# Kernel optimization log

Measured on AMD Instinct MI355X. Metric: run time of the kernel, lower is better.

The kernel has to match this reference:

```python
import jax, jax.numpy as jnp
import numpy as np

H = 12  # num_heads (init kwarg)


def setup_inputs() -> dict:
    key = jax.random.key(0)
    ks = jax.random.split(key, 9)
    B, S, D, M = 2, 1025, 768, 4
    hw = S - 1
    x = jax.random.normal(ks[0], (B, S, D), dtype=jnp.float32)
    masks = jax.random.randint(ks[1], (B, M, hw), 0, 2, dtype=jnp.int32)
    init = lambda k: jax.random.normal(k, (D, D), dtype=jnp.float32) * 0.02
    return {
        'x': x, 'masks': masks,
        'Wq': init(ks[2]), 'bq': jnp.zeros((D,), jnp.float32),
        'Wk': init(ks[3]), 'bk': jnp.zeros((D,), jnp.float32),
        'Wv': init(ks[4]), 'bv': jnp.zeros((D,), jnp.float32),
    }


def reference(x, masks, Wq, bq, Wk, bk, Wv, bv):
    B, S, D = x.shape
    hd = D // H
    scale = 1.0 / jnp.sqrt(jnp.asarray(hd, x.dtype))

    def heads(t):  # (B,S,D) -> (B,H,S,hd)
        return t.reshape(B, S, H, hd).transpose(0, 2, 1, 3)

    q = heads(x @ Wq.T + bq)
    k = heads(x @ Wk.T + bk)
    v = heads(x @ Wv.T + bv)

    scores_ori = jnp.einsum('bhqd,bhkd->bhqk', q, k) * scale  # (B,H,S,S)
    attn = jax.nn.softmax(scores_ori, axis=-1)  # dropout is identity at eval
    h = jnp.einsum('bhqk,bhkd->bhqd', attn, v)
    h = h.transpose(0, 2, 1, 3).reshape(B, S, D)

    # ---- mask-expanded attention (torch.no_grad branch) ----
    Mk, hw = masks.shape[1], masks.shape[2]
    m = masks.astype(x.dtype)  # (B,M,hw)
    # pad: position 0 (CLS) gets 0, positions 1..hw get the mask
    new_masks = jnp.pad(m, ((0, 0), (0, 0), (1, S - 1 - hw)))  # (B,M,S)
    bias = -10000.0 * (1.0 - new_masks)  # additive mask bias
    new_scores = scores_ori[:, None] + bias[:, :, None, None, :]  # (B,M,H,S,S)
    new_attn = jax.nn.softmax(new_scores, axis=-1)
    new_h = jnp.einsum('bmhqk,bhkd->bmhqd', new_attn, v)  # v repeated per mask
    new_h = new_h.transpose(0, 1, 3, 2, 4).reshape(B * Mk, S, D)

    img_idx = jnp.repeat(jnp.arange(B), Mk)  # [0]*M + [1]*M + ...
    new_x = jnp.broadcast_to(x[:, None], (B, Mk, S, D)).reshape(B * Mk, S, D)
    return (h, new_h, img_idx, new_x)
```

## Files before the change

kernel.cpp:

```cpp
#include <hip/hip_runtime.h>

typedef float f32x4 __attribute__((ext_vector_type(4)));
typedef short s16x8 __attribute__((ext_vector_type(8)));

constexpr int B  = 2;
constexpr int S  = 1025;
constexpr int D  = 768;
constexpr int DD = D * D;
constexpr int H  = 12;
constexpr int NM = 4;
constexpr int ROWS = B * S;
constexpr int BSD  = B * S * D;
constexpr int KPAD = 1088;
constexpr int NHB  = B * H;
constexpr int NQT  = 65;
constexpr int NKT  = 17;
constexpr int NV5  = 5;
constexpr int NATT = NHB * NQT;
constexpr int NCPY = 512;
constexpr int OUT_NEWH_OFF = BSD;
constexpr int OUT_IDX_OFF  = BSD + NM * BSD;
constexpr int OUT_NEWX_OFF = OUT_IDX_OFF + B * NM;

#define QSCALE 0.18033688011112042f

constexpr size_t QF_SZ = (size_t)NHB * NQT * 2 * 512;
constexpr size_t KF_SZ = (size_t)NHB * NKT * 4 * 2 * 512;
constexpr size_t VF_SZ = KF_SZ;

__device__ __forceinline__ unsigned short f2bf(float f) {
    unsigned u = __builtin_bit_cast(unsigned, f);
    u += 0x7FFF + ((u >> 16) & 1);
    return (unsigned short)(u >> 16);
}

__device__ __forceinline__ void gll16(const void* g, void* l) {
    __builtin_amdgcn_global_load_lds(
        (const __attribute__((address_space(1))) void*)g,
        (__attribute__((address_space(3))) void*)l, 16, 0, 0);
}

__global__ __launch_bounds__(256) void conv_kernel(
    const float* __restrict__ x, const float* __restrict__ Wq,
    const float* __restrict__ Wk, const float* __restrict__ Wv,
    const int* __restrict__ masks,
    unsigned short* __restrict__ xb, unsigned short* __restrict__ Wb,
    unsigned short* __restrict__ Mmb,
    unsigned short* __restrict__ Qf, unsigned short* __restrict__ Kf,
    unsigned short* __restrict__ Vf)
{
    constexpr int NX8 = BSD / 8;
    constexpr int NW8 = DD / 8;
    constexpr int TOT = NX8 + 3 * NW8;
    const int stride = gridDim.x * 256;
    const int tid = blockIdx.x * 256 + threadIdx.x;
    for (int c = tid; c < TOT; c += stride) {
        const float* src;
        unsigned short* dst;
        if (c < NX8) { src = x + (size_t)c * 8; dst = xb + (size_t)c * 8; }
        else {
            const int cc = c - NX8;
            const int mt = cc / NW8;
            const int rr = cc - mt * NW8;
            src = ((mt == 0) ? Wq : (mt == 1) ? Wk : Wv) + (size_t)rr * 8;
            dst = Wb + (size_t)mt * DD + (size_t)rr * 8;
        }
        const float4 a = *(const float4*)src;
        const float4 b2 = *(const float4*)(src + 4);
        s16x8 v;
        v[0] = (short)f2bf(a.x);  v[1] = (short)f2bf(a.y);
        v[2] = (short)f2bf(a.z);  v[3] = (short)f2bf(a.w);
        v[4] = (short)f2bf(b2.x); v[5] = (short)f2bf(b2.y);
        v[6] = (short)f2bf(b2.z); v[7] = (short)f2bf(b2.w);
        *(s16x8*)dst = v;
    }
    if (tid < B * NV5 * KPAD) {
        const int k    = tid % KPAD;
        const int rest = tid / KPAD;
        const int vv   = rest % NV5;
        const int bb   = rest / NV5;
        unsigned short m;
        if (vv == 0) m = (k < S) ? 0xFFFFu : 0u;
        else m = (k >= 1 && k < S &&
                  masks[(size_t)(bb * NM + vv - 1) * (S - 1) + k - 1]) ? 0xFFFFu : 0u;
        Mmb[tid] = m;
    }
    constexpr int KZ = NHB * 8 * 512;
    for (int i = tid; i < KZ; i += stride) {
        const int hb = i >> 12, off = i & 4095;
        Kf[(((size_t)(hb * NKT + NKT - 1)) << 12) + off] = 0;
        Vf[(((size_t)(hb * NKT + NKT - 1)) << 12) + off] = 0;
    }
    constexpr int QZ = NHB * 2 * 512;
    for (int i = tid; i < QZ; i += stride) {
        const int hb = i >> 10, off = i & 1023;
        Qf[(((size_t)(hb * NQT + NQT - 1) * 2) << 9) + off] = 0;
    }
}

__global__ __launch_bounds__(256, 2) void qkv_mfma_kernel(
    const unsigned short* __restrict__ xb, const unsigned short* __restrict__ Wb,
    const float* __restrict__ bq, const float* __restrict__ bk,
    const float* __restrict__ bv,
    unsigned short* __restrict__ Qf, unsigned short* __restrict__ Kf,
    unsigned short* __restrict__ Vf)
{
    __shared__ __align__(16) unsigned short Xs[2][128 * 64];
    __shared__ __align__(16) unsigned short Wl[2][128 * 64];

    const int t = threadIdx.x;
    const int row0 = blockIdx.x * 128;
    const int cy = blockIdx.y;
    const int mt = cy / 6;
    const int col0 = (cy % 6) * 128;
    const float* bias = (mt == 0) ? bq : (mt == 1) ? bk : bv;
    const unsigned short* Wsrc = Wb + (size_t)mt * DD;

    const int w = t >> 6, l = t & 63, lq = l & 15, grp = l >> 4;
    const int wr = w >> 1, wc = w & 1;

    auto stage = [&](int buf, int k0) {
        #pragma unroll
        for (int i = 0; i < 4; ++i) {
            const int slot = i * 256 + t;
            const int r = slot >> 3, cl = slot & 7;
            const int cg = cl ^ (r & 7);
            int row = row0 + r; if (row > ROWS - 1) row = ROWS - 1;
            gll16(xb + (size_t)row * D + k0 + cg * 8, &Xs[buf][slot * 8]);
            gll16(Wsrc + (size_t)(col0 + r) * D + k0 + cg * 8, &Wl[buf][slot * 8]);
        }
    };

    f32x4 acc[4][4] = {};
    stage(0, 0);

    for (int ks = 0; ks < 12; ++ks) {
        const int cur = ks & 1;
        __syncthreads();
        if (ks + 1 < 12) stage(cur ^ 1, (ks + 1) * 64);

        s16x8 a[4][2], bf[4][2];
        #pragma unroll
        for (int i = 0; i < 4; ++i) {
            const int xr = wr * 64 + i * 16 + lq;
            #pragma unroll
            for (int kh = 0; kh < 2; ++kh)
                a[i][kh] = *(const s16x8*)&Xs[cur][xr * 64 + (((kh * 4 + grp) ^ (xr & 7)) * 8)];
        }
        #pragma unroll
        for (int j = 0; j < 4; ++j) {
            const int wrow = wc * 64 + j * 16 + lq;
            #pragma unroll
            for (int kh = 0; kh < 2; ++kh)
                bf[j][kh] = *(const s16x8*)&Wl[cur][wrow * 64 + (((kh * 4 + grp) ^ (wrow & 7)) * 8)];
        }
        #pragma unroll
        for (int i = 0; i < 4; ++i)
            #pragma unroll
            for (int j = 0; j < 4; ++j) {
                acc[i][j] = __builtin_amdgcn_mfma_f32_16x16x32_bf16(a[i][0], bf[j][0], acc[i][j], 0, 0, 0);
                acc[i][j] = __builtin_amdgcn_mfma_f32_16x16x32_bf16(a[i][1], bf[j][1], acc[i][j], 0, 0, 0);
            }
    }

    #pragma unroll
    for (int j = 0; j < 4; ++j) {
        const int col = col0 + wc * 64 + j * 16 + lq;
        const float bv_ = bias[col];
        #pragma unroll
        for (int i = 0; i < 4; ++i) {
            #pragma unroll
            for (int r = 0; r < 4; ++r) {
                const int row = row0 + wr * 64 + i * 16 + grp * 4 + r;
                if (row >= ROWS) continue;
                const float raw = acc[i][j][r] + bv_;
                const int bb = (row >= S) ? 1 : 0;
                const int s  = row - bb * S;
                const int hb2 = bb * H + (col >> 6);
                const int d   = col & 63;
                if (mt == 0) {
                    const size_t idx = (((size_t)(hb2 * NQT + (s >> 4)) * 2 + (d >> 5)) << 9)
                                     + (((((d >> 3) & 3) << 4) + (s & 15)) << 3) + (d & 7);
                    Qf[idx] = f2bf(raw * QSCALE);
                } else if (mt == 1) {
                    const size_t idx = ((((size_t)(hb2 * NKT + (s >> 6)) * 4 + ((s >> 4) & 3)) * 2 + (d >> 5)) << 9)
                                     + (((((d >> 3) & 3) << 4) + (s & 15)) << 3) + (d & 7);
                    Kf[idx] = f2bf(raw);
                } else {
                    const int kk = s & 63;
                    const size_t idx = ((((size_t)(hb2 * NKT + (s >> 6)) * 4 + (d >> 4)) * 2 + (kk >> 5)) << 9)
                                     + (((((kk >> 3) & 3) << 4) + (d & 15)) << 3) + (kk & 7);
                    Vf[idx] = f2bf(raw);
                }
            }
        }
    }
}

__global__ __launch_bounds__(384) void attn_mfma_kernel(
    const unsigned short* __restrict__ Qf, const unsigned short* __restrict__ Kf,
    const unsigned short* __restrict__ Vf, const unsigned short* __restrict__ Mmb,
    const float* __restrict__ x,
    float* __restrict__ out_h, float* __restrict__ out_newh,
    float* __restrict__ out_newx, float* __restrict__ out_idx)
{
    if (blockIdx.x >= NATT) {
        const int cb = blockIdx.x - NATT;
        const int SLAB4  = S * D / 4;
        const int TOTAL4 = B * NM * SLAB4;
        const float4* x4 = (const float4*)x;
        float4* o4 = (float4*)out_newx;
        for (int f = cb * 384 + threadIdx.x; f < TOTAL4; f += NCPY * 384) {
            const int bm  = f / SLAB4;
            const int rem = f - bm * SLAB4;
            o4[f] = x4[(bm >> 2) * SLAB4 + rem];
        }
        if (cb == 0 && threadIdx.x < B * NM)
            out_idx[threadIdx.x] = (float)(threadIdx.x >> 2);
        return;
    }

    __shared__ __align__(16) unsigned short KVl[2][2][4096];
    __shared__ __align__(16) unsigned short Pb2[2][1024];

    const int orig = blockIdx.x;
    const int wgid = (orig & 7) * 195 + (orig >> 3);
    const int hb = wgid / NQT;
    const int qt = wgid - hb * NQT;
    const int b  = hb / H, hh = hb - b * H;
    const int q0 = qt * 16;

    const int t = threadIdx.x;
    const int w = t >> 6, l = t & 63;
    const int lq = l & 15, grp = l >> 4;

    const unsigned short* kfT = Kf + (((size_t)(hb * NKT)) << 12);
    const unsigned short* vfT = Vf + (((size_t)(hb * NKT)) << 12);

    auto stage = [&](int buf, int tile) {
        const unsigned short* ks = kfT + ((size_t)tile << 12);
        const unsigned short* vs = vfT + ((size_t)tile << 12);
        #pragma unroll
        for (int i = 0; i < 3; ++i) {
            const int s = t + i * 384;
            if (s < 512)       gll16(ks + s * 8, &KVl[buf][0][s * 8]);
            else if (s < 1024) gll16(vs + (s - 512) * 8, &KVl[buf][1][(s - 512) * 8]);
        }
    };

    stage(0, 0);

    if (w == 0) {
        s16x8 qf0, qf1;
        {
            const unsigned short* p = Qf + (((size_t)(hb * NQT + qt) * 2) << 9) + (l << 3);
            qf0 = *(const s16x8*)p;
            qf1 = *(const s16x8*)(p + 512);
        }
        #pragma unroll
        for (int it = 0; it < NKT; ++it) {
            const int cur = it & 1;
            __syncthreads();
            if (it + 1 < NKT) stage(cur ^ 1, it + 1);

            s16x8 kf[4][2];
            #pragma unroll
            for (int kt = 0; kt < 4; ++kt)
                #pragma unroll
                for (int kh = 0; kh < 2; ++kh)
                    kf[kt][kh] = *(const s16x8*)&KVl[cur][0][((kt * 2 + kh) << 9) + l * 8];

            f32x4 qk[4] = {};
            __builtin_amdgcn_s_setprio(1);
            #pragma unroll
            for (int kt = 0; kt < 4; ++kt) {
                qk[kt] = __builtin_amdgcn_mfma_f32_16x16x32_bf16(kf[kt][0], qf0, qk[kt], 0, 0, 0);
                qk[kt] = __builtin_amdgcn_mfma_f32_16x16x32_bf16(kf[kt][1], qf1, qk[kt], 0, 0, 0);
            }
            __builtin_amdgcn_s_setprio(0);

            unsigned short* P = &Pb2[cur][0];
            #pragma unroll
            for (int kt = 0; kt < 4; ++kt) {
                float e0, e1, e2, e3;
                asm("v_exp_f32 %0, %1" : "=v"(e0) : "v"(qk[kt][0]));
                asm("v_exp_f32 %0, %1" : "=v"(e1) : "v"(qk[kt][1]));
                asm("v_exp_f32 %0, %1" : "=v"(e2) : "v"(qk[kt][2]));
                asm("v_exp_f32 %0, %1" : "=v"(e3) : "v"(qk[kt][3]));
                unsigned d0, d1;
                asm("v_cvt_pk_bf16_f32 %0, %1, %2" : "=v"(d0) : "v"(e0), "v"(e1));
                asm("v_cvt_pk_bf16_f32 %0, %1, %2" : "=v"(d1) : "v"(e2), "v"(e3));
                const int chunk = kt * 2 + (grp >> 1);
                *(uint2*)&P[lq * 64 + ((chunk ^ (lq & 7)) * 8) + (grp & 1) * 4] =
                    make_uint2(d0, d1);
            }
        }
        __syncthreads();
    } else {
        const int vv = w - 1;
        const unsigned short* mbase = Mmb + (size_t)(b * NV5 + vv) * KPAD + grp * 8;

        s16x8 onesf;
        #pragma unroll
        for (int i = 0; i < 8; ++i) onesf[i] = (short)0x3F80;

        f32x4 acc[5] = {};
        s16x8 vfp[4][2];

        auto pv = [&](s16x8 ea0, s16x8 ea1, int mi) {
            s16x8 mm0 = *(const s16x8*)(mbase + mi * 64);
            s16x8 mm1 = *(const s16x8*)(mbase + mi * 64 + 32);
            s16x8 pa0 = ea0 & mm0;
            s16x8 pa1 = ea1 & mm1;
            __builtin_amdgcn_s_setprio(1);
            #pragma unroll
            for (int dt = 0; dt < 4; ++dt)
                acc[dt] = __builtin_amdgcn_mfma_f32_16x16x32_bf16(vfp[dt][0], pa0, acc[dt], 0, 0, 0);
            acc[4] = __builtin_amdgcn_mfma_f32_16x16x32_bf16(onesf, pa0, acc[4], 0, 0, 0);
            #pragma unroll
            for (int dt = 0; dt < 4; ++dt)
                acc[dt] = __builtin_amdgcn_mfma_f32_16x16x32_bf16(vfp[dt][1], pa1, acc[dt], 0, 0, 0);
            acc[4] = __builtin_amdgcn_mfma_f32_16x16x32_bf16(onesf, pa1, acc[4], 0, 0, 0);
            __builtin_amdgcn_s_setprio(0);
        };

        #pragma unroll
        for (int it = 0; it < NKT; ++it) {
            const int cur = it & 1;
            __syncthreads();
            if (it + 1 < NKT) stage(cur ^ 1, it + 1);

            s16x8 pr0, pr1;
            if (it > 0) {
                const unsigned short* Pr = &Pb2[cur ^ 1][0];
                pr0 = *(const s16x8*)&Pr[lq * 64 + ((grp ^ (lq & 7)) * 8)];
                pr1 = *(const s16x8*)&Pr[lq * 64 + (((4 + grp) ^ (lq & 7)) * 8)];
            }
            s16x8 vfc[4][2];
            #pragma unroll
            for (int dt = 0; dt < 4; ++dt)
                #pragma unroll
                for (int kh = 0; kh < 2; ++kh)
                    vfc[dt][kh] = *(const s16x8*)&KVl[cur][1][((dt * 2 + kh) << 9) + l * 8];

            if (it > 0) pv(pr0, pr1, it - 1);

            #pragma unroll
            for (int dt = 0; dt < 4; ++dt) {
                vfp[dt][0] = vfc[dt][0];
                vfp[dt][1] = vfc[dt][1];
            }
        }
        __syncthreads();
        {
            const unsigned short* Pr = &Pb2[(NKT - 1) & 1][0];
            s16x8 pr0 = *(const s16x8*)&Pr[lq * 64 + ((grp ^ (lq & 7)) * 8)];
            s16x8 pr1 = *(const s16x8*)&Pr[lq * 64 + (((4 + grp) ^ (lq & 7)) * 8)];
            pv(pr0, pr1, NKT - 1);
        }

        const int q = q0 + lq;
        if (q < S) {
            const float inv = 1.0f / acc[4][0];
            float* bp = ((vv == 0)
                ? out_h    + (size_t)(b * S + q) * D
                : out_newh + (size_t)((b * NM + vv - 1) * S + q) * D) + hh * 64 + grp * 4;
            #pragma unroll
            for (int dt = 0; dt < 4; ++dt) {
                float4 s4;
                s4.x = acc[dt][0] * inv; s4.y = acc[dt][1] * inv;
                s4.z = acc[dt][2] * inv; s4.w = acc[dt][3] * inv;
                *(float4*)(bp + dt * 16) = s4;
            }
        }
    }
}

extern "C" void kernel_launch(void* const* d_in, const int* in_sizes, int n_in,
                              void* d_out, int out_size, void* d_ws, size_t ws_size,
                              hipStream_t stream)
{
    const float* x     = (const float*)d_in[0];
    const int*   masks = (const int*)  d_in[1];
    const float* Wq    = (const float*)d_in[2];
    const float* bq    = (const float*)d_in[3];
    const float* Wk    = (const float*)d_in[4];
    const float* bk    = (const float*)d_in[5];
    const float* Wv    = (const float*)d_in[6];
    const float* bv    = (const float*)d_in[7];

    float* out = (float*)d_out;
    float* out_h    = out;
    float* out_newh = out + OUT_NEWH_OFF;
    float* out_idx  = out + OUT_IDX_OFF;
    float* out_newx = out + OUT_NEWX_OFF;

    unsigned short* Qf  = (unsigned short*)d_ws;
    unsigned short* Kf  = Qf + QF_SZ;
    unsigned short* Vf  = Kf + KF_SZ;
    unsigned short* Mmb = Vf + VF_SZ;

    unsigned short* xb = (unsigned short*)out_newx;
    unsigned short* Wb = xb + BSD;

    conv_kernel<<<1634, 256, 0, stream>>>(x, Wq, Wk, Wv, masks, xb, Wb, Mmb,
                                          Qf, Kf, Vf);
    {
        dim3 grid(17, 18);
        qkv_mfma_kernel<<<grid, 256, 0, stream>>>(xb, Wb, bq, bk, bv, Qf, Kf, Vf);
    }
    attn_mfma_kernel<<<NATT + NCPY, 384, 0, stream>>>(Qf, Kf, Vf, Mmb, x,
                                                      out_h, out_newh,
                                                      out_newx, out_idx);
}
```

Before: 96.71 us.

## Split PV work by head-dim slice per wave, loading V fragments directly from global

Waves 1-4 each compute one 16-wide slice of the head dimension for all five mask variants, instead of each wave computing the full head dimension for one variant. A dedicated wave 5 computes the row sums for all variants and publishes them through shared memory. V is no longer staged in LDS; each wave reads its own V fragments straight from global memory, which halves the staged LDS traffic. The row sums now need an extra barrier, and the V loads become uncached global reads on the critical path.

```diff
diff --git a/kernel.cpp b/kernel.cpp
--- a/kernel.cpp
+++ b/kernel.cpp
@@ -220,8 +220,9 @@
         return;
     }
 
-    __shared__ __align__(16) unsigned short KVl[2][2][4096];
+    __shared__ __align__(16) unsigned short Kl[2][4096];
     __shared__ __align__(16) unsigned short Pb2[2][1024];
+    __shared__ float Ssum[NV5][16];
 
     const int orig = blockIdx.x;
     const int wgid = (orig & 7) * 195 + (orig >> 3);
@@ -235,16 +236,13 @@
     const int lq = l & 15, grp = l >> 4;
 
     const unsigned short* kfT = Kf + (((size_t)(hb * NKT)) << 12);
-    const unsigned short* vfT = Vf + (((size_t)(hb * NKT)) << 12);
 
     auto stage = [&](int buf, int tile) {
         const unsigned short* ks = kfT + ((size_t)tile << 12);
-        const unsigned short* vs = vfT + ((size_t)tile << 12);
-        #pragma unroll
-        for (int i = 0; i < 3; ++i) {
+        #pragma unroll
+        for (int i = 0; i < 2; ++i) {
             const int s = t + i * 384;
-            if (s < 512)       gll16(ks + s * 8, &KVl[buf][0][s * 8]);
-            else if (s < 1024) gll16(vs + (s - 512) * 8, &KVl[buf][1][(s - 512) * 8]);
+            if (s < 512) gll16(ks + s * 8, &Kl[buf][s * 8]);
         }
     };
 
@@ -257,25 +255,20 @@
             qf0 = *(const s16x8*)p;
             qf1 = *(const s16x8*)(p + 512);
         }
-        #pragma unroll
+        #pragma unroll 1
         for (int it = 0; it < NKT; ++it) {
             const int cur = it & 1;
             __syncthreads();
             if (it + 1 < NKT) stage(cur ^ 1, it + 1);
 
-            s16x8 kf[4][2];
-            #pragma unroll
-            for (int kt = 0; kt < 4; ++kt)
-                #pragma unroll
-                for (int kh = 0; kh < 2; ++kh)
-                    kf[kt][kh] = *(const s16x8*)&KVl[cur][0][((kt * 2 + kh) << 9) + l * 8];
-
             f32x4 qk[4] = {};
             __builtin_amdgcn_s_setprio(1);
             #pragma unroll
             for (int kt = 0; kt < 4; ++kt) {
-                qk[kt] = __builtin_amdgcn_mfma_f32_16x16x32_bf16(kf[kt][0], qf0, qk[kt], 0, 0, 0);
-                qk[kt] = __builtin_amdgcn_mfma_f32_16x16x32_bf16(kf[kt][1], qf1, qk[kt], 0, 0, 0);
+                s16x8 k0v = *(const s16x8*)&Kl[cur][((kt * 2 + 0) << 9) + l * 8];
+                s16x8 k1v = *(const s16x8*)&Kl[cur][((kt * 2 + 1) << 9) + l * 8];
+                qk[kt] = __builtin_amdgcn_mfma_f32_16x16x32_bf16(k0v, qf0, qk[kt], 0, 0, 0);
+                qk[kt] = __builtin_amdgcn_mfma_f32_16x16x32_bf16(k1v, qf1, qk[kt], 0, 0, 0);
             }
             __builtin_amdgcn_s_setprio(0);
 
@@ -296,35 +289,16 @@
             }
         }
         __syncthreads();
-    } else {
-        const int vv = w - 1;
-        const unsigned short* mbase = Mmb + (size_t)(b * NV5 + vv) * KPAD + grp * 8;
-
-        s16x8 onesf;
-        #pragma unroll
-        for (int i = 0; i < 8; ++i) onesf[i] = (short)0x3F80;
-
-        f32x4 acc[5] = {};
-        s16x8 vfp[4][2];
-
-        auto pv = [&](s16x8 ea0, s16x8 ea1, int mi) {
-            s16x8 mm0 = *(const s16x8*)(mbase + mi * 64);
-            s16x8 mm1 = *(const s16x8*)(mbase + mi * 64 + 32);
-            s16x8 pa0 = ea0 & mm0;
-            s16x8 pa1 = ea1 & mm1;
-            __builtin_amdgcn_s_setprio(1);
-            #pragma unroll
-            for (int dt = 0; dt < 4; ++dt)
-                acc[dt] = __builtin_amdgcn_mfma_f32_16x16x32_bf16(vfp[dt][0], pa0, acc[dt], 0, 0, 0);
-            acc[4] = __builtin_amdgcn_mfma_f32_16x16x32_bf16(onesf, pa0, acc[4], 0, 0, 0);
-            #pragma unroll
-            for (int dt = 0; dt < 4; ++dt)
-                acc[dt] = __builtin_amdgcn_mfma_f32_16x16x32_bf16(vfp[dt][1], pa1, acc[dt], 0, 0, 0);
-            acc[4] = __builtin_amdgcn_mfma_f32_16x16x32_bf16(onesf, pa1, acc[4], 0, 0, 0);
-            __builtin_amdgcn_s_setprio(0);
-        };
-
-        #pragma unroll
+        __syncthreads();
+    } else if (w <= 4) {
+        const int dt = w - 1;
+        const unsigned short* mball = Mmb + (size_t)(b * NV5) * KPAD + grp * 8;
+        const unsigned short* vfb = Vf + (((size_t)(hb * NKT)) << 12) + (l << 3);
+
+        f32x4 acc[NV5] = {};
+        s16x8 vfp0, vfp1;
+
+        #pragma unroll 1
         for (int it = 0; it < NKT; ++it) {
             const int cur = it & 1;
             __syncthreads();
@@ -336,43 +310,101 @@
                 pr0 = *(const s16x8*)&Pr[lq * 64 + ((grp ^ (lq & 7)) * 8)];
                 pr1 = *(const s16x8*)&Pr[lq * 64 + (((4 + grp) ^ (lq & 7)) * 8)];
             }
-            s16x8 vfc[4][2];
-            #pragma unroll
-            for (int dt = 0; dt < 4; ++dt)
+            s16x8 nv0 = *(const s16x8*)&vfb[((size_t)(it * 8 + dt * 2 + 0)) << 9];
+            s16x8 nv1 = *(const s16x8*)&vfb[((size_t)(it * 8 + dt * 2 + 1)) << 9];
+
+            if (it > 0) {
+                const int mi = it - 1;
+                __builtin_amdgcn_s_setprio(1);
                 #pragma unroll
-                for (int kh = 0; kh < 2; ++kh)
-                    vfc[dt][kh] = *(const s16x8*)&KVl[cur][1][((dt * 2 + kh) << 9) + l * 8];
-
-            if (it > 0) pv(pr0, pr1, it - 1);
-
-            #pragma unroll
-            for (int dt = 0; dt < 4; ++dt) {
-                vfp[dt][0] = vfc[dt][0];
-                vfp[dt][1] = vfc[dt][1];
-            }
+                for (int v = 0; v < NV5; ++v) {
+                    s16x8 mm0 = *(const s16x8*)(mball + (size_t)v * KPAD + mi * 64);
+                    s16x8 mm1 = *(const s16x8*)(mball + (size_t)v * KPAD + mi * 64 + 32);
+                    acc[v] = __builtin_amdgcn_mfma_f32_16x16x32_bf16(vfp0, pr0 & mm0, acc[v], 0, 0, 0);
+                    acc[v] = __builtin_amdgcn_mfma_f32_16x16x32_bf16(vfp1, pr1 & mm1, acc[v], 0, 0, 0);
+                }
+                __builtin_amdgcn_s_setprio(0);
+            }
+            vfp0 = nv0; vfp1 = nv1;
         }
         __syncthreads();
         {
-            const unsigned short* Pr = &Pb2[(NKT - 1) & 1][0];
+            const int mi = NKT - 1;
+            const unsigned short* Pr = &Pb2[mi & 1][0];
             s16x8 pr0 = *(const s16x8*)&Pr[lq * 64 + ((grp ^ (lq & 7)) * 8)];
             s16x8 pr1 = *(const s16x8*)&Pr[lq * 64 + (((4 + grp) ^ (lq & 7)) * 8)];
-            pv(pr0, pr1, NKT - 1);
-        }
+            #pragma unroll
+            for (int v = 0; v < NV5; ++v) {
+                s16x8 mm0 = *(const s16x8*)(mball + (size_t)v * KPAD + mi * 64);
+                s16x8 mm1 = *(const s16x8*)(mball + (size_t)v * KPAD + mi * 64 + 32);
+                acc[v] = __builtin_amdgcn_mfma_f32_16x16x32_bf16(vfp0, pr0 & mm0, acc[v], 0, 0, 0);
+                acc[v] = __builtin_amdgcn_mfma_f32_16x16x32_bf16(vfp1, pr1 & mm1, acc[v], 0, 0, 0);
+            }
+        }
+        __syncthreads();
 
         const int q = q0 + lq;
         if (q < S) {
-            const float inv = 1.0f / acc[4][0];
-            float* bp = ((vv == 0)
-                ? out_h    + (size_t)(b * S + q) * D
-                : out_newh + (size_t)((b * NM + vv - 1) * S + q) * D) + hh * 64 + grp * 4;
-            #pragma unroll
-            for (int dt = 0; dt < 4; ++dt) {
+            #pragma unroll
+            for (int v = 0; v < NV5; ++v) {
+                const float inv = 1.0f / Ssum[v][lq];
+                float* bp = ((v == 0)
+                    ? out_h    + (size_t)(b * S + q) * D
+                    : out_newh + (size_t)((b * NM + v - 1) * S + q) * D)
+                    + hh * 64 + dt * 16 + grp * 4;
                 float4 s4;
-                s4.x = acc[dt][0] * inv; s4.y = acc[dt][1] * inv;
-                s4.z = acc[dt][2] * inv; s4.w = acc[dt][3] * inv;
-                *(float4*)(bp + dt * 16) = s4;
-            }
-        }
+                s4.x = acc[v][0] * inv; s4.y = acc[v][1] * inv;
+                s4.z = acc[v][2] * inv; s4.w = acc[v][3] * inv;
+                *(float4*)bp = s4;
+            }
+        }
+    } else {
+        const unsigned short* mball = Mmb + (size_t)(b * NV5) * KPAD + grp * 8;
+        s16x8 onesf;
+        #pragma unroll
+        for (int i = 0; i < 8; ++i) onesf[i] = (short)0x3F80;
+
+        f32x4 accs[NV5] = {};
+
+        #pragma unroll 1
+        for (int it = 0; it < NKT; ++it) {
+            const int cur = it & 1;
+            __syncthreads();
+            if (it + 1 < NKT) stage(cur ^ 1, it + 1);
+
+            if (it > 0) {
+                const unsigned short* Pr = &Pb2[cur ^ 1][0];
+                s16x8 pr0 = *(const s16x8*)&Pr[lq * 64 + ((grp ^ (lq & 7)) * 8)];
+                s16x8 pr1 = *(const s16x8*)&Pr[lq * 64 + (((4 + grp) ^ (lq & 7)) * 8)];
+                const int mi = it - 1;
+                #pragma unroll
+                for (int v = 0; v < NV5; ++v) {
+                    s16x8 mm0 = *(const s16x8*)(mball + (size_t)v * KPAD + mi * 64);
+                    s16x8 mm1 = *(const s16x8*)(mball + (size_t)v * KPAD + mi * 64 + 32);
+                    accs[v] = __builtin_amdgcn_mfma_f32_16x16x32_bf16(onesf, pr0 & mm0, accs[v], 0, 0, 0);
+                    accs[v] = __builtin_amdgcn_mfma_f32_16x16x32_bf16(onesf, pr1 & mm1, accs[v], 0, 0, 0);
+                }
+            }
+        }
+        __syncthreads();
+        {
+            const int mi = NKT - 1;
+            const unsigned short* Pr = &Pb2[mi & 1][0];
+            s16x8 pr0 = *(const s16x8*)&Pr[lq * 64 + ((grp ^ (lq & 7)) * 8)];
+            s16x8 pr1 = *(const s16x8*)&Pr[lq * 64 + (((4 + grp) ^ (lq & 7)) * 8)];
+            #pragma unroll
+            for (int v = 0; v < NV5; ++v) {
+                s16x8 mm0 = *(const s16x8*)(mball + (size_t)v * KPAD + mi * 64);
+                s16x8 mm1 = *(const s16x8*)(mball + (size_t)v * KPAD + mi * 64 + 32);
+                accs[v] = __builtin_amdgcn_mfma_f32_16x16x32_bf16(onesf, pr0 & mm0, accs[v], 0, 0, 0);
+                accs[v] = __builtin_amdgcn_mfma_f32_16x16x32_bf16(onesf, pr1 & mm1, accs[v], 0, 0, 0);
+            }
+        }
+        if (grp == 0) {
+            #pragma unroll
+            for (int v = 0; v < NV5; ++v) Ssum[v][lq] = accs[v][0];
+        }
+        __syncthreads();
     }
 }
 
```

After: 135.1 us. +39.7%, slower.
